# Performance work log

Measured on AMD Instinct MI355X. Metric: run time of the kernel, lower is better.

## Reference

```python
import math
import jax, jax.numpy as jnp
import numpy as np

SQ = 5  # locality window width (static, from init_kwargs)

def _locality_mask_np(hidden_size: int, width: int) -> np.ndarray:
    """[H, H] 0/1 mask: units live on a side x side grid; unit i connects to
    unit j iff their circular (wrap-around) Chebyshev grid distance <= width//2.
    mask_type='circular' -> toroidal wrap."""
    side = int(round(math.sqrt(hidden_size)))
    assert side * side == hidden_size
    r = np.arange(hidden_size) // side
    c = np.arange(hidden_size) % side
    dr = np.abs(r[:, None] - r[None, :])
    dc = np.abs(c[:, None] - c[None, :])
    dr = np.minimum(dr, side - dr)  # circular wrap
    dc = np.minimum(dc, side - dc)
    half = width // 2
    return ((dr <= half) & (dc <= half)).astype(np.float32)


def setup_inputs() -> dict:
    key = jax.random.key(0)
    ks = jax.random.split(key, 8)
    B, S, H = 8, 2048, 1024
    scale = 0.02
    x = jax.random.normal(ks[0], (B, S, H), dtype=jnp.float32)
    Wq = jax.random.normal(ks[1], (H, H), dtype=jnp.float32) * scale
    Wk = jax.random.normal(ks[2], (H, H), dtype=jnp.float32) * scale
    Wv = jax.random.normal(ks[3], (H, H), dtype=jnp.float32) * scale
    bq = jnp.zeros((H,), dtype=jnp.float32)
    bk = jnp.zeros((H,), dtype=jnp.float32)
    bv = jnp.zeros((H,), dtype=jnp.float32)
    Wl = jax.random.normal(ks[4], (H, H), dtype=jnp.float32) * scale
    return {"x": x, "Wq": Wq, "bq": bq, "Wk": Wk, "bk": bk,
            "Wv": Wv, "bv": bv, "Wl": Wl}


def reference(x, Wq, bq, Wk, bk, Wv, bv, Wl):
    H = x.shape[-1]
    mask = jnp.asarray(_locality_mask_np(H, SQ))  # [H, H], static
    # Locally-connected q/k/v projections: dense weight elementwise-masked.
    q = x @ (Wq * mask).T + bq  # [B, S, H]
    k = x @ (Wk * mask).T + bk
    v = x @ (Wv * mask).T + bv
    # Learned spatial querying: locality-masked learned map applied to query.
    q = q @ (Wl * mask).T  # [B, S, H]
    # Manual attention (dropout is identity in eval / p=0).
    scores = jnp.einsum("bsh,bth->bst", q, k) / math.sqrt(H)  # [B, S, S]
    probs = jax.nn.softmax(scores, axis=-1)
    out = jnp.einsum("bst,bth->bsh", probs, v)  # [B, S, H]
    return out, probs
```

## Files before the change

### kernel.cpp

```cpp
#include <hip/hip_runtime.h>

typedef __attribute__((ext_vector_type(8))) short short8;
typedef __attribute__((ext_vector_type(4))) float floatx4;

__device__ __forceinline__ unsigned short f2bf(float f) {
  union { float f; unsigned int u; } x; x.f = f;
  unsigned int r = (x.u + 0x7fffu + ((x.u >> 16) & 1u)) >> 16;
  return (unsigned short)r;
}
__device__ __forceinline__ float bf2f(unsigned short u) {
  union { unsigned int u; float f; } x; x.u = ((unsigned int)u) << 16;
  return x.f;
}

__device__ __forceinline__ void gload_lds16(const void* g, void* l) {
  __builtin_amdgcn_global_load_lds((const __attribute__((address_space(1))) void*)g,
                                   (__attribute__((address_space(3))) void*)l,
                                   16, 0, 0);
}

__global__ __launch_bounds__(128) void prep_weights(
    const float* __restrict__ Wq, const float* __restrict__ Wk,
    const float* __restrict__ Wv, const float* __restrict__ Wl,
    const float* __restrict__ bq, const float* __restrict__ bk,
    const float* __restrict__ bv,
    unsigned short* __restrict__ Wqkv, float* __restrict__ biasAll) {
  const int i = blockIdx.x;
  const int r = i >> 5, c = i & 31;
  const int t = threadIdx.x;
  for (int p = t; p < 1024; p += 128) {
    Wqkv[i * 1024 + p] = 0;
    Wqkv[(1024 + i) * 1024 + p] = 0;
    Wqkv[(2048 + i) * 1024 + p] = 0;
  }
  __syncthreads();
  if (t < 25) {
    int dr = t / 5 - 2, dc = t % 5 - 2;
    int j = (((r + dr) & 31) << 5) | ((c + dc) & 31);
    Wqkv[(1024 + i) * 1024 + j] = f2bf(Wk[i * 1024 + j]);
    Wqkv[(2048 + i) * 1024 + j] = f2bf(Wv[i * 1024 + j]);
  }
  if (t < 81) {
    int dr = t / 9 - 4, dc = t % 9 - 4;
    int j = (((r + dr) & 31) << 5) | ((c + dc) & 31);
    float s = 0.f;
    int erlo = dr - 2 < -2 ? -2 : dr - 2, erhi = dr + 2 > 2 ? 2 : dr + 2;
    int eclo = dc - 2 < -2 ? -2 : dc - 2, echi = dc + 2 > 2 ? 2 : dc + 2;
    for (int er = erlo; er <= erhi; ++er)
      for (int ec = eclo; ec <= echi; ++ec) {
        int m = (((r + er) & 31) << 5) | ((c + ec) & 31);
        s += Wl[i * 1024 + m] * Wq[m * 1024 + j];
      }
    Wqkv[i * 1024 + j] = f2bf(s);
  }
  if (t == 96) {
    float s = 0.f;
    for (int e = 0; e < 25; ++e) {
      int dr = e / 5 - 2, dc = e % 5 - 2;
      int m = (((r + dr) & 31) << 5) | ((c + dc) & 31);
      s += Wl[i * 1024 + m] * bq[m];
    }
    biasAll[i] = s;
  }
  if (t == 97) biasAll[1024 + i] = bk[i];
  if (t == 98) biasAll[2048 + i] = bv[i];
}

__global__ __launch_bounds__(256) void cast_bf16(const float4* __restrict__ x,
                                                 ushort4* __restrict__ xb) {
  int i = blockIdx.x * 256 + threadIdx.x;
  float4 v = x[i];
  ushort4 o;
  o.x = f2bf(v.x); o.y = f2bf(v.y); o.z = f2bf(v.z); o.w = f2bf(v.w);
  xb[i] = o;
}

template <int OUTMODE>
__global__ __launch_bounds__(512, 2) void gemm256(
    const unsigned short* __restrict__ A, const unsigned short* __restrict__ B,
    void* __restrict__ Cv, const float* __restrict__ auxc, float* __restrict__ auxw,
    int lda, int ldb, int ldc, int K, float scale,
    size_t sA, size_t sB, size_t sC) {
  __shared__ __align__(16) unsigned short lds[65536];
  const int t = threadIdx.x;
  const int lane = t & 63;
  const int wv = t >> 6;
  const int wm = wv >> 2;
  const int wn = wv & 3;
  const int l15 = lane & 15, lq = lane >> 4;
  const int bm = blockIdx.y, bn = blockIdx.x, bz = blockIdx.z;
  A += sA * bz; B += sB * bz;

  const int rl = t >> 3;
  const int gd = (t & 7) ^ (rl & 7);
  const int wb = (t >> 6) << 9;

#define STAGE_A(q, tt_)                                                        \
  gload_lds16(A + (size_t)(bm * 256 + (q) * 64 + rl) * lda + (tt_) * 64 + gd * 8, \
              &lds[(((tt_) & 1) << 14) + ((q) << 12) + wb])
#define STAGE_B(q, tt_)                                                        \
  gload_lds16(B + (size_t)(bn * 256 + (q) * 64 + rl) * ldb + (tt_) * 64 + gd * 8, \
              &lds[32768 + (((tt_) & 1) << 14) + ((q) << 12) + wb])

  floatx4 acc[8][4];
#pragma unroll
  for (int i = 0; i < 8; ++i)
#pragma unroll
    for (int j = 0; j < 4; ++j) acc[i][j] = (floatx4){0.f, 0.f, 0.f, 0.f};

  const int NT = K >> 6;

  STAGE_A(0, 0); STAGE_A(1, 0); STAGE_A(2, 0); STAGE_A(3, 0);
  STAGE_B(0, 0); STAGE_B(1, 0); STAGE_B(2, 0); STAGE_B(3, 0);
  asm volatile("" ::: "memory");
  STAGE_A(0, 1); STAGE_A(2, 1);
  asm volatile("s_waitcnt vmcnt(2)" ::: "memory");
  __builtin_amdgcn_s_barrier();

  for (int tt = 0; tt < NT; ++tt) {
    const int bo = (tt & 1) << 14;
    short8 aF[4][2], bFa[2][2], bFb[2][2];

#pragma unroll
    for (int i = 0; i < 4; ++i) {
      int rA = wm * 128 + i * 16 + l15;
#pragma unroll
      for (int ks = 0; ks < 2; ++ks) {
        int g = ks * 4 + lq;
        aF[i][ks] = *(const short8*)&lds[bo + rA * 64 + ((g ^ (rA & 7)) << 3)];
      }
    }
#pragma unroll
    for (int j = 0; j < 2; ++j) {
      int rB = wn * 64 + j * 16 + l15;
#pragma unroll
      for (int ks = 0; ks < 2; ++ks) {
        int g = ks * 4 + lq;
        bFa[j][ks] = *(const short8*)&lds[32768 + bo + rB * 64 + ((g ^ (rB & 7)) << 3)];
      }
    }
    if (tt + 1 < NT) { STAGE_A(1, tt + 1); STAGE_A(3, tt + 1); STAGE_B(2, tt + 1); STAGE_B(3, tt + 1); }
    __builtin_amdgcn_s_barrier();
    __builtin_amdgcn_s_setprio(1);
#pragma unroll
    for (int i = 0; i < 4; ++i)
#pragma unroll
      for (int j = 0; j < 2; ++j) {
        acc[i][j] = __builtin_amdgcn_mfma_f32_16x16x32_bf16(aF[i][0], bFa[j][0], acc[i][j], 0, 0, 0);
        acc[i][j] = __builtin_amdgcn_mfma_f32_16x16x32_bf16(aF[i][1], bFa[j][1], acc[i][j], 0, 0, 0);
      }
    __builtin_amdgcn_s_setprio(0);
    asm volatile("s_waitcnt lgkmcnt(0)" ::: "memory");
    __builtin_amdgcn_s_barrier();

#pragma unroll
    for (int j = 0; j < 2; ++j) {
      int rB = wn * 64 + 32 + j * 16 + l15;
#pragma unroll
      for (int ks = 0; ks < 2; ++ks) {
        int g = ks * 4 + lq;
        bFb[j][ks] = *(const short8*)&lds[32768 + bo + rB * 64 + ((g ^ (rB & 7)) << 3)];
      }
    }
    if (tt + 1 < NT) { STAGE_B(0, tt + 1); STAGE_B(1, tt + 1); }
    __builtin_amdgcn_s_barrier();
    __builtin_amdgcn_s_setprio(1);
#pragma unroll
    for (int i = 0; i < 4; ++i)
#pragma unroll
      for (int j = 0; j < 2; ++j) {
        acc[i][2 + j] = __builtin_amdgcn_mfma_f32_16x16x32_bf16(aF[i][0], bFb[j][0], acc[i][2 + j], 0, 0, 0);
        acc[i][2 + j] = __builtin_amdgcn_mfma_f32_16x16x32_bf16(aF[i][1], bFb[j][1], acc[i][2 + j], 0, 0, 0);
      }
    __builtin_amdgcn_s_setprio(0);
    asm volatile("s_waitcnt lgkmcnt(0)" ::: "memory");
    __builtin_amdgcn_s_barrier();

#pragma unroll
    for (int i = 0; i < 4; ++i) {
      int rA = wm * 128 + 64 + i * 16 + l15;
#pragma unroll
      for (int ks = 0; ks < 2; ++ks) {
        int g = ks * 4 + lq;
        aF[i][ks] = *(const short8*)&lds[bo + rA * 64 + ((g ^ (rA & 7)) << 3)];
      }
    }
    if (tt + 2 < NT) { STAGE_A(0, tt + 2); STAGE_A(2, tt + 2); }
    __builtin_amdgcn_s_barrier();
    __builtin_amdgcn_s_setprio(1);
#pragma unroll
    for (int i = 0; i < 4; ++i)
#pragma unroll
      for (int j = 0; j < 2; ++j) {
        acc[4 + i][2 + j] = __builtin_amdgcn_mfma_f32_16x16x32_bf16(aF[i][0], bFb[j][0], acc[4 + i][2 + j], 0, 0, 0);
        acc[4 + i][2 + j] = __builtin_amdgcn_mfma_f32_16x16x32_bf16(aF[i][1], bFb[j][1], acc[4 + i][2 + j], 0, 0, 0);
      }
    __builtin_amdgcn_s_setprio(0);
    asm volatile("s_waitcnt lgkmcnt(0)" ::: "memory");
    __builtin_amdgcn_s_barrier();

    __builtin_amdgcn_s_setprio(1);
#pragma unroll
    for (int i = 0; i < 4; ++i)
#pragma unroll
      for (int j = 0; j < 2; ++j) {
        acc[4 + i][j] = __builtin_amdgcn_mfma_f32_16x16x32_bf16(aF[i][0], bFa[j][0], acc[4 + i][j], 0, 0, 0);
        acc[4 + i][j] = __builtin_amdgcn_mfma_f32_16x16x32_bf16(aF[i][1], bFa[j][1], acc[4 + i][j], 0, 0, 0);
      }
    __builtin_amdgcn_s_setprio(0);
    if (tt < NT - 2)       { asm volatile("s_waitcnt vmcnt(2)" ::: "memory"); }
    else if (tt == NT - 2) { asm volatile("s_waitcnt vmcnt(0)" ::: "memory"); }
    __builtin_amdgcn_s_barrier();
  }
#undef STAGE_A
#undef STAGE_B

  const int row0 = bm * 256 + wm * 128;
  const int col0 = bn * 256 + wn * 64;

  if (OUTMODE == 0) {
    unsigned short* C = (unsigned short*)Cv + sC * bz;
#pragma unroll
    for (int m = 0; m < 8; ++m) {
      int rb = row0 + ((m >> 2) << 6) + ((m & 3) << 4) + (lq << 2);
#pragma unroll
      for (int n = 0; n < 4; ++n) {
        int col = col0 + ((n >> 1) << 5) + ((n & 1) << 4) + l15;
        float bb = auxc[col];
#pragma unroll
        for (int r2 = 0; r2 < 4; ++r2)
          C[(size_t)(rb + r2) * ldc + col] = f2bf(acc[m][n][r2] + bb);
      }
    }
  } else if (OUTMODE == 2) {
    unsigned short* C = (unsigned short*)Cv + sC * bz;
    float p[8][4];
#pragma unroll
    for (int m = 0; m < 8; ++m)
#pragma unroll
      for (int r2 = 0; r2 < 4; ++r2) p[m][r2] = 0.f;
#pragma unroll
    for (int m = 0; m < 8; ++m) {
      int rb = row0 + ((m >> 2) << 6) + ((m & 3) << 4) + (lq << 2);
#pragma unroll
      for (int n = 0; n < 4; ++n) {
        int col = col0 + ((n >> 1) << 5) + ((n & 1) << 4) + l15;
#pragma unroll
        for (int r2 = 0; r2 < 4; ++r2) {
          float e = __expf(acc[m][n][r2] * scale);
          C[(size_t)(rb + r2) * ldc + col] = f2bf(e);
          p[m][r2] += e;
        }
      }
    }
#pragma unroll
    for (int m = 0; m < 8; ++m)
#pragma unroll
      for (int r2 = 0; r2 < 4; ++r2) {
        float v = p[m][r2];
        v += __shfl_xor(v, 1); v += __shfl_xor(v, 2);
        v += __shfl_xor(v, 4); v += __shfl_xor(v, 8);
        p[m][r2] = v;
      }
    float* sred = (float*)lds;
    if (l15 == 0) {
#pragma unroll
      for (int m = 0; m < 8; ++m)
#pragma unroll
        for (int r2 = 0; r2 < 4; ++r2)
          sred[wn * 256 + wm * 128 + ((m >> 2) << 6) + ((m & 3) << 4) + (lq << 2) + r2] = p[m][r2];
    }
    __syncthreads();
    if (t < 256) {
      float L = sred[t] + sred[256 + t] + sred[512 + t] + sred[768 + t];
      auxw[((size_t)bz * 2048 + bm * 256 + t) * 8 + bn] = L;
    }
  } else {
    float* C = (float*)Cv + sC * bz;
#pragma unroll
    for (int m = 0; m < 8; ++m) {
      int rb = row0 + ((m >> 2) << 6) + ((m & 3) << 4) + (lq << 2);
      float il[4];
#pragma unroll
      for (int r2 = 0; r2 < 4; ++r2)
        il[r2] = auxc[(size_t)bz * 2048 + rb + r2];
#pragma unroll
      for (int n = 0; n < 4; ++n) {
        int col = col0 + ((n >> 1) << 5) + ((n & 1) << 4) + l15;
#pragma unroll
        for (int r2 = 0; r2 < 4; ++r2)
          C[(size_t)(rb + r2) * ldc + col] = acc[m][n][r2] * il[r2];
      }
    }
  }
}

__global__ __launch_bounds__(1024) void transpose_v(const unsigned short* __restrict__ qkv,
                                                    unsigned short* __restrict__ vT) {
  __shared__ unsigned short tile[32][33];
  int s0 = blockIdx.x * 32, h0 = blockIdx.y * 32, b = blockIdx.z;
  int tx = threadIdx.x, ty = threadIdx.y;
  tile[ty][tx] = qkv[((size_t)b * 2048 + s0 + ty) * 3072 + 2048 + h0 + tx];
  __syncthreads();
  vT[((size_t)b * 1024 + h0 + ty) * 2048 + s0 + tx] = tile[tx][ty];
}

__global__ __launch_bounds__(256) void finish_softmax(
    const float* __restrict__ Lpart, const unsigned short* __restrict__ pb,
    float* __restrict__ invL, float* __restrict__ probs) {
  const size_t row = blockIdx.x;
  const int t = threadIdx.x;
  __shared__ float sInv;
  if (t < 64) {
    float s = (t < 8) ? Lpart[row * 8 + t] : 0.f;
    s += __shfl_xor(s, 1); s += __shfl_xor(s, 2); s += __shfl_xor(s, 4);
    if (t == 0) {
      float inv = 1.0f / s;
      sInv = inv;
      invL[row] = inv;
    }
  }
  __syncthreads();
  float inv = sInv;
  const ushort4* pv = (const ushort4*)(pb + row * 2048);
  float4* pr = (float4*)(probs + row * 2048);
  ushort4 a = pv[t * 2], b = pv[t * 2 + 1];
  float4 o0, o1;
  o0.x = bf2f(a.x) * inv; o0.y = bf2f(a.y) * inv;
  o0.z = bf2f(a.z) * inv; o0.w = bf2f(a.w) * inv;
  o1.x = bf2f(b.x) * inv; o1.y = bf2f(b.y) * inv;
  o1.z = bf2f(b.z) * inv; o1.w = bf2f(b.w) * inv;
  pr[t * 2] = o0; pr[t * 2 + 1] = o1;
}

extern "C" void kernel_launch(void* const* d_in, const int* in_sizes, int n_in,
                              void* d_out, int out_size, void* d_ws, size_t ws_size,
                              hipStream_t stream) {
  const float* x  = (const float*)d_in[0];
  const float* Wq = (const float*)d_in[1];
  const float* bq = (const float*)d_in[2];
  const float* Wk = (const float*)d_in[3];
  const float* bk = (const float*)d_in[4];
  const float* Wv = (const float*)d_in[5];
  const float* bv = (const float*)d_in[6];
  const float* Wl = (const float*)d_in[7];

  const int B = 8, S = 2048, H = 1024;
  float* out   = (float*)d_out;
  float* probs = (float*)d_out + (size_t)B * S * H;

  char* ws = (char*)d_ws;
  unsigned short* qkv  = (unsigned short*)(ws + 0);
  unsigned short* pb   = (unsigned short*)(ws + 100663296);
  unsigned short* xb   = (unsigned short*)(ws + 167772160);
  unsigned short* vT   = (unsigned short*)(ws + 167772160);
  unsigned short* Wqkv = (unsigned short*)(ws + 201326592);
  float* biasAll       = (float*)(ws + 207618048);
  float* Lpart         = (float*)(ws + 207630336);
  float* invL          = (float*)(ws + 208678912);

  prep_weights<<<1024, 128, 0, stream>>>(Wq, Wk, Wv, Wl, bq, bk, bv, Wqkv, biasAll);
  cast_bf16<<<16384, 256, 0, stream>>>((const float4*)x, (ushort4*)xb);

  gemm256<0><<<dim3(12, 64, 1), 512, 0, stream>>>(xb, Wqkv, qkv, biasAll, nullptr,
      H, H, 3 * H, H, 1.f, 0, 0, 0);

  transpose_v<<<dim3(64, 32, 8), dim3(32, 32), 0, stream>>>(qkv, vT);

  gemm256<2><<<dim3(8, 8, 8), 512, 0, stream>>>(qkv, qkv + 1024, pb, nullptr, Lpart,
      3 * H, 3 * H, S, H, 1.0f / 32.0f, (size_t)S * 3 * H, (size_t)S * 3 * H, (size_t)S * S);

  finish_softmax<<<16384, 256, 0, stream>>>(Lpart, pb, invL, probs);

  gemm256<3><<<dim3(4, 8, 8), 512, 0, stream>>>(pb, vT, out, invL, nullptr,
      S, S, H, S, 1.0f, (size_t)S * S, (size_t)H * S, (size_t)S * H);
}
```

Before: 550.3 us.

## Restage GEMM loads by half-tile with 2x unrolled loop; vectorize V transpose

The GEMM main loop is unrolled by two so the double-buffer offsets become compile-time constants. Global-to-LDS staging is regrouped into 128-row halves, with the next tiles' loads interleaved across the MFMA phases and new vmcnt wait thresholds. The V transpose now has each thread move four bf16 values through a 32x33 tile with ushort4 loads and stores, using 256-thread blocks. This aims to cut address arithmetic and get earlier prefetch overlap, but the hand-tuned waitcnt counts must exactly match the issue order or the kernel will race.

```diff
diff --git a/kernel.cpp b/kernel.cpp
--- a/kernel.cpp
+++ b/kernel.cpp
@@ -91,16 +91,46 @@
   const int bm = blockIdx.y, bn = blockIdx.x, bz = blockIdx.z;
   A += sA * bz; B += sB * bz;
 
-  const int rl = t >> 3;
-  const int gd = (t & 7) ^ (rl & 7);
-  const int wb = (t >> 6) << 9;
-
-#define STAGE_A(q, tt_)                                                        \
-  gload_lds16(A + (size_t)(bm * 256 + (q) * 64 + rl) * lda + (tt_) * 64 + gd * 8, \
-              &lds[(((tt_) & 1) << 14) + ((q) << 12) + wb])
-#define STAGE_B(q, tt_)                                                        \
-  gload_lds16(B + (size_t)(bn * 256 + (q) * 64 + rl) * ldb + (tt_) * 64 + gd * 8, \
-              &lds[32768 + (((tt_) & 1) << 14) + ((q) << 12) + wb])
+  const int srow = t >> 3;
+  const int sg = (t & 7) ^ (srow & 7);
+
+#define STG_A(h, tile_) do {                                                     \
+    gload_lds16(A + (size_t)(bm * 256 + (h) * 128 + srow) * lda + (tile_) * 64 + sg * 8, \
+                &lds[(((tile_) & 1) << 14) + (h) * 8192 + wv * 512]);            \
+    gload_lds16(A + (size_t)(bm * 256 + (h) * 128 + 64 + srow) * lda + (tile_) * 64 + sg * 8, \
+                &lds[(((tile_) & 1) << 14) + (h) * 8192 + 4096 + wv * 512]);     \
+  } while (0)
+#define STG_B(h, tile_) do {                                                     \
+    gload_lds16(B + (size_t)(bn * 256 + (h) * 128 + srow) * ldb + (tile_) * 64 + sg * 8, \
+                &lds[32768 + (((tile_) & 1) << 14) + (h) * 8192 + wv * 512]);    \
+    gload_lds16(B + (size_t)(bn * 256 + (h) * 128 + 64 + srow) * ldb + (tile_) * 64 + sg * 8, \
+                &lds[32768 + (((tile_) & 1) << 14) + (h) * 8192 + 4096 + wv * 512]); \
+  } while (0)
+
+#define LOADA(arr, ro)                                                           \
+  _Pragma("unroll") for (int i = 0; i < 4; ++i) {                                \
+    int rA = wm * 128 + (ro) + i * 16 + l15;                                     \
+    _Pragma("unroll") for (int ks = 0; ks < 2; ++ks)                             \
+      arr[i][ks] = *(const short8*)&lds[bo_ + rA * 64 + (((ks * 4 + lq) ^ (rA & 7)) << 3)]; \
+  }
+#define LOADB(arr, ro)                                                           \
+  _Pragma("unroll") for (int j = 0; j < 2; ++j) {                                \
+    int rB = wn * 64 + (ro) + j * 16 + l15;                                      \
+    _Pragma("unroll") for (int ks = 0; ks < 2; ++ks)                             \
+      arr[j][ks] = *(const short8*)&lds[32768 + bo_ + rB * 64 + (((ks * 4 + lq) ^ (rB & 7)) << 3)]; \
+  }
+#define MFMA8(mb, nb, aa, bb)                                                    \
+  _Pragma("unroll") for (int i = 0; i < 4; ++i)                                  \
+    _Pragma("unroll") for (int j = 0; j < 2; ++j) {                              \
+      acc[(mb) + i][(nb) + j] = __builtin_amdgcn_mfma_f32_16x16x32_bf16(         \
+          aa[i][0], bb[j][0], acc[(mb) + i][(nb) + j], 0, 0, 0);                 \
+      acc[(mb) + i][(nb) + j] = __builtin_amdgcn_mfma_f32_16x16x32_bf16(         \
+          aa[i][1], bb[j][1], acc[(mb) + i][(nb) + j], 0, 0, 0);                 \
+    }
+#define FENCE asm volatile("" ::: "memory")
+#define BAR __builtin_amdgcn_s_barrier()
+#define SP1 __builtin_amdgcn_s_setprio(1)
+#define SP0 __builtin_amdgcn_s_setprio(0)
 
   floatx4 acc[8][4];
 #pragma unroll
@@ -110,110 +140,66 @@
 
   const int NT = K >> 6;
 
-  STAGE_A(0, 0); STAGE_A(1, 0); STAGE_A(2, 0); STAGE_A(3, 0);
-  STAGE_B(0, 0); STAGE_B(1, 0); STAGE_B(2, 0); STAGE_B(3, 0);
-  asm volatile("" ::: "memory");
-  STAGE_A(0, 1); STAGE_A(2, 1);
-  asm volatile("s_waitcnt vmcnt(2)" ::: "memory");
-  __builtin_amdgcn_s_barrier();
-
-  for (int tt = 0; tt < NT; ++tt) {
-    const int bo = (tt & 1) << 14;
+  STG_A(0, 0); STG_A(1, 0); STG_B(0, 0); STG_B(1, 0);
+  FENCE;
+  STG_B(0, 1); STG_A(0, 1); STG_B(1, 1);
+  asm volatile("s_waitcnt vmcnt(6)" ::: "memory");
+  BAR;
+
+  for (int T = 0; T < NT; T += 2) {
     short8 aF[4][2], bFa[2][2], bFb[2][2];
-
-#pragma unroll
-    for (int i = 0; i < 4; ++i) {
-      int rA = wm * 128 + i * 16 + l15;
-#pragma unroll
-      for (int ks = 0; ks < 2; ++ks) {
-        int g = ks * 4 + lq;
-        aF[i][ks] = *(const short8*)&lds[bo + rA * 64 + ((g ^ (rA & 7)) << 3)];
-      }
-    }
-#pragma unroll
-    for (int j = 0; j < 2; ++j) {
-      int rB = wn * 64 + j * 16 + l15;
-#pragma unroll
-      for (int ks = 0; ks < 2; ++ks) {
-        int g = ks * 4 + lq;
-        bFa[j][ks] = *(const short8*)&lds[32768 + bo + rB * 64 + ((g ^ (rB & 7)) << 3)];
-      }
-    }
-    if (tt + 1 < NT) { STAGE_A(1, tt + 1); STAGE_A(3, tt + 1); STAGE_B(2, tt + 1); STAGE_B(3, tt + 1); }
-    __builtin_amdgcn_s_barrier();
-    __builtin_amdgcn_s_setprio(1);
-#pragma unroll
-    for (int i = 0; i < 4; ++i)
-#pragma unroll
-      for (int j = 0; j < 2; ++j) {
-        acc[i][j] = __builtin_amdgcn_mfma_f32_16x16x32_bf16(aF[i][0], bFa[j][0], acc[i][j], 0, 0, 0);
-        acc[i][j] = __builtin_amdgcn_mfma_f32_16x16x32_bf16(aF[i][1], bFa[j][1], acc[i][j], 0, 0, 0);
-      }
-    __builtin_amdgcn_s_setprio(0);
-    asm volatile("s_waitcnt lgkmcnt(0)" ::: "memory");
-    __builtin_amdgcn_s_barrier();
-
-#pragma unroll
-    for (int j = 0; j < 2; ++j) {
-      int rB = wn * 64 + 32 + j * 16 + l15;
-#pragma unroll
-      for (int ks = 0; ks < 2; ++ks) {
-        int g = ks * 4 + lq;
-        bFb[j][ks] = *(const short8*)&lds[32768 + bo + rB * 64 + ((g ^ (rB & 7)) << 3)];
-      }
-    }
-    if (tt + 1 < NT) { STAGE_B(0, tt + 1); STAGE_B(1, tt + 1); }
-    __builtin_amdgcn_s_barrier();
-    __builtin_amdgcn_s_setprio(1);
-#pragma unroll
-    for (int i = 0; i < 4; ++i)
-#pragma unroll
-      for (int j = 0; j < 2; ++j) {
-        acc[i][2 + j] = __builtin_amdgcn_mfma_f32_16x16x32_bf16(aF[i][0], bFb[j][0], acc[i][2 + j], 0, 0, 0);
-        acc[i][2 + j] = __builtin_amdgcn_mfma_f32_16x16x32_bf16(aF[i][1], bFb[j][1], acc[i][2 + j], 0, 0, 0);
-      }
-    __builtin_amdgcn_s_setprio(0);
-    asm volatile("s_waitcnt lgkmcnt(0)" ::: "memory");
-    __builtin_amdgcn_s_barrier();
-
-#pragma unroll
-    for (int i = 0; i < 4; ++i) {
-      int rA = wm * 128 + 64 + i * 16 + l15;
-#pragma unroll
-      for (int ks = 0; ks < 2; ++ks) {
-        int g = ks * 4 + lq;
-        aF[i][ks] = *(const short8*)&lds[bo + rA * 64 + ((g ^ (rA & 7)) << 3)];
-      }
-    }
-    if (tt + 2 < NT) { STAGE_A(0, tt + 2); STAGE_A(2, tt + 2); }
-    __builtin_amdgcn_s_barrier();
-    __builtin_amdgcn_s_setprio(1);
-#pragma unroll
-    for (int i = 0; i < 4; ++i)
-#pragma unroll
-      for (int j = 0; j < 2; ++j) {
-        acc[4 + i][2 + j] = __builtin_amdgcn_mfma_f32_16x16x32_bf16(aF[i][0], bFb[j][0], acc[4 + i][2 + j], 0, 0, 0);
-        acc[4 + i][2 + j] = __builtin_amdgcn_mfma_f32_16x16x32_bf16(aF[i][1], bFb[j][1], acc[4 + i][2 + j], 0, 0, 0);
-      }
-    __builtin_amdgcn_s_setprio(0);
-    asm volatile("s_waitcnt lgkmcnt(0)" ::: "memory");
-    __builtin_amdgcn_s_barrier();
-
-    __builtin_amdgcn_s_setprio(1);
-#pragma unroll
-    for (int i = 0; i < 4; ++i)
-#pragma unroll
-      for (int j = 0; j < 2; ++j) {
-        acc[4 + i][j] = __builtin_amdgcn_mfma_f32_16x16x32_bf16(aF[i][0], bFa[j][0], acc[4 + i][j], 0, 0, 0);
-        acc[4 + i][j] = __builtin_amdgcn_mfma_f32_16x16x32_bf16(aF[i][1], bFa[j][1], acc[4 + i][j], 0, 0, 0);
-      }
-    __builtin_amdgcn_s_setprio(0);
-    if (tt < NT - 2)       { asm volatile("s_waitcnt vmcnt(2)" ::: "memory"); }
-    else if (tt == NT - 2) { asm volatile("s_waitcnt vmcnt(0)" ::: "memory"); }
-    __builtin_amdgcn_s_barrier();
-  }
-#undef STAGE_A
-#undef STAGE_B
+    {
+      const int bo_ = 0;
+      LOADA(aF, 0); LOADB(bFa, 0);
+      STG_A(1, T + 1);
+      FENCE; BAR;
+      SP1; MFMA8(0, 0, aF, bFa); SP0;
+      FENCE; BAR;
+      LOADB(bFb, 32);
+      FENCE; BAR;
+      SP1; MFMA8(0, 2, aF, bFb); SP0;
+      FENCE; BAR;
+      LOADA(aF, 64);
+      if (T + 2 < NT) STG_B(0, T + 2);
+      FENCE; BAR;
+      SP1; MFMA8(4, 2, aF, bFb); SP0;
+      FENCE; BAR;
+      if (T + 2 < NT) STG_A(0, T + 2);
+      FENCE; BAR;
+      SP1; MFMA8(4, 0, aF, bFa); SP0;
+      if (T + 2 < NT) { asm volatile("s_waitcnt vmcnt(4)" ::: "memory"); }
+      else            { asm volatile("s_waitcnt vmcnt(0)" ::: "memory"); }
+      FENCE; BAR;
+    }
+    {
+      const int bo_ = 1 << 14;
+      LOADA(aF, 0); LOADB(bFa, 0);
+      if (T + 2 < NT) { STG_B(1, T + 2); STG_A(1, T + 2); }
+      FENCE; BAR;
+      SP1; MFMA8(0, 0, aF, bFa); SP0;
+      FENCE; BAR;
+      LOADB(bFb, 32);
+      FENCE; BAR;
+      SP1; MFMA8(0, 2, aF, bFb); SP0;
+      FENCE; BAR;
+      LOADA(aF, 64);
+      if (T + 3 < NT) STG_B(0, T + 3);
+      FENCE; BAR;
+      SP1; MFMA8(4, 2, aF, bFb); SP0;
+      FENCE; BAR;
+      if (T + 3 < NT) { STG_A(0, T + 3); STG_B(1, T + 3); }
+      FENCE; BAR;
+      SP1; MFMA8(4, 0, aF, bFa); SP0;
+      if (T + 3 < NT) { asm volatile("s_waitcnt vmcnt(6)" ::: "memory"); }
+      else            { asm volatile("s_waitcnt vmcnt(0)" ::: "memory"); }
+      FENCE; BAR;
+    }
+  }
+#undef STG_A
+#undef STG_B
+#undef LOADA
+#undef LOADB
+#undef MFMA8
 
   const int row0 = bm * 256 + wm * 128;
   const int col0 = bn * 256 + wn * 64;
@@ -295,14 +281,21 @@
   }
 }
 
-__global__ __launch_bounds__(1024) void transpose_v(const unsigned short* __restrict__ qkv,
-                                                    unsigned short* __restrict__ vT) {
+__global__ __launch_bounds__(256) void transpose_v(const unsigned short* __restrict__ qkv,
+                                                   unsigned short* __restrict__ vT) {
   __shared__ unsigned short tile[32][33];
   int s0 = blockIdx.x * 32, h0 = blockIdx.y * 32, b = blockIdx.z;
-  int tx = threadIdx.x, ty = threadIdx.y;
-  tile[ty][tx] = qkv[((size_t)b * 2048 + s0 + ty) * 3072 + 2048 + h0 + tx];
+  int tx = threadIdx.x;
+  int ty = threadIdx.y;
+  ushort4 v = *(const ushort4*)&qkv[((size_t)b * 2048 + s0 + ty) * 3072 + 2048 + h0 + tx * 4];
+  int c0 = tx * 4;
+  tile[ty][c0 + 0] = v.x; tile[ty][c0 + 1] = v.y;
+  tile[ty][c0 + 2] = v.z; tile[ty][c0 + 3] = v.w;
   __syncthreads();
-  vT[((size_t)b * 1024 + h0 + ty) * 2048 + s0 + tx] = tile[tx][ty];
+  ushort4 o;
+  o.x = tile[c0 + 0][ty]; o.y = tile[c0 + 1][ty];
+  o.z = tile[c0 + 2][ty]; o.w = tile[c0 + 3][ty];
+  *(ushort4*)&vT[((size_t)b * 1024 + h0 + ty) * 2048 + s0 + c0] = o;
 }
 
 __global__ __launch_bounds__(256) void finish_softmax(
@@ -365,7 +358,7 @@
   gemm256<0><<<dim3(12, 64, 1), 512, 0, stream>>>(xb, Wqkv, qkv, biasAll, nullptr,
       H, H, 3 * H, H, 1.f, 0, 0, 0);
 
-  transpose_v<<<dim3(64, 32, 8), dim3(32, 32), 0, stream>>>(qkv, vT);
+  transpose_v<<<dim3(64, 32, 8), dim3(8, 32), 0, stream>>>(qkv, vT);
 
   gemm256<2><<<dim3(8, 8, 8), 512, 0, stream>>>(qkv, qkv + 1024, pb, nullptr, Lpart,
       3 * H, 3 * H, S, H, 1.0f / 32.0f, (size_t)S * 3 * H, (size_t)S * 3 * H, (size_t)S * S);
```

Measured after the change: 541.3 us. Within noise of the previous version (-1.6%).
